# Performance work log

Hardware: AMD Instinct MI355X
Metric: run time of the kernel (lower is better)

The kernel has to match this reference:

```python
import jax, jax.numpy as jnp
import numpy as np

D = 256
H = 8
HD = D // H  # 32
EPS = 1e-5


def _ln(x, g, b):
    m = jnp.mean(x, axis=-1, keepdims=True)
    v = jnp.var(x, axis=-1, keepdims=True)
    return (x - m) * jax.lax.rsqrt(v + EPS) * g + b


def setup_inputs() -> dict:
    key = jax.random.key(0)
    ks = jax.random.split(key, 30)
    B = 131072
    s = 0.05

    def w(k, shape, scale=s):
        return jax.random.normal(k, shape, dtype=jnp.float32) * scale

    inp = {
        'f24': w(ks[0], (B, D), 1.0),
        'f77': w(ks[1], (B, D), 1.0),
        'fx': w(ks[2], (B, D), 1.0),
        'norm_g': jnp.ones((D,), jnp.float32),
        'norm_b': jnp.zeros((D,), jnp.float32),
        'Wq24': w(ks[3], (D, D)), 'bq24': w(ks[4], (D,)),
        'Wk24': w(ks[5], (D, D)), 'bk24': w(ks[6], (D,)),
        'Wv24': w(ks[7], (D, D)), 'bv24': w(ks[8], (D,)),
        'Wq77': w(ks[9], (D, D)), 'bq77': w(ks[10], (D,)),
        'Wk77': w(ks[11], (D, D)), 'bk77': w(ks[12], (D,)),
        'Wv77': w(ks[13], (D, D)), 'bv77': w(ks[14], (D,)),
        'Wqx': w(ks[15], (D, D)), 'bqx': w(ks[16], (D,)),
        'Wkx': w(ks[17], (D, D)), 'bkx': w(ks[18], (D,)),
        'Wvx': w(ks[19], (D, D)), 'bvx': w(ks[20], (D,)),
        'Wout': w(ks[21], (D, D)), 'bout': w(ks[22], (D,)),
        'radar_w': jnp.ones((3,), jnp.float32),
        'W1': w(ks[23], (D, 4 * D)), 'b1': w(ks[24], (4 * D,)),
        'W2': w(ks[25], (4 * D, D)), 'b2': w(ks[26], (D,)),
        'fnorm_g': jnp.ones((D,), jnp.float32),
        'fnorm_b': jnp.zeros((D,), jnp.float32),
    }
    return inp


def reference(f24, f77, fx, norm_g, norm_b,
              Wq24, bq24, Wk24, bk24, Wv24, bv24,
              Wq77, bq77, Wk77, bk77, Wv77, bv77,
              Wqx, bqx, Wkx, bkx, Wvx, bvx,
              Wout, bout, radar_w, W1, b1, W2, b2,
              fnorm_g, fnorm_b):
    B = f24.shape[0]
    residual = (f24 + f77 + fx) / 3.0
    n24 = _ln(f24, norm_g, norm_b)
    n77 = _ln(f77, norm_g, norm_b)
    nx = _ln(fx, norm_g, norm_b)

    def proj(x, W, b):
        return (x @ W + b).reshape(B, H, HD)

    q24 = proj(n24, Wq24, bq24); k24 = proj(n24, Wk24, bk24); v24 = proj(n24, Wv24, bv24)
    q77 = proj(n77, Wq77, bq77); k77 = proj(n77, Wk77, bk77); v77 = proj(n77, Wv77, bv77)
    qx = proj(nx, Wqx, bqx); kx = proj(nx, Wkx, bkx); vx = proj(nx, Wvx, bvx)

    scale = HD ** (-0.5)

    def att(q, ka, kb):  # [B,H,H] each
        a = jnp.einsum('bhd,bgd->bhg', q, ka) * scale
        b_ = jnp.einsum('bhd,bgd->bhg', q, kb) * scale
        # softmax across the two radar sources (stacked dim), NOT over keys
        return jax.nn.softmax(jnp.stack([a, b_], axis=1), axis=1)

    attn_24 = att(q24, k77, kx)
    attn_77 = att(q77, k24, kx)
    attn_x = att(qx, k24, k77)

    def mix(p, va, vb):  # [B,2,H,H] x [B,H,HD] -> [B, D]
        o = jnp.einsum('bhg,bgd->bhd', p[:, 0], va) + jnp.einsum('bhg,bgd->bhd', p[:, 1], vb)
        return o.reshape(B, D)

    out_24 = mix(attn_24, v77, vx)
    out_77 = mix(attn_77, v24, vx)
    out_x = mix(attn_x, v24, v77)

    rw = jax.nn.softmax(radar_w, axis=0)
    fused = rw[0] * out_24 + rw[1] * out_77 + rw[2] * out_x
    fused = fused @ Wout + bout
    fused = fused + residual
    ff = jax.nn.gelu(fused @ W1 + b1, approximate=False) @ W2 + b2  # dropout = eval identity
    output = _ln(fused + ff, fnorm_g, fnorm_b)
    return output, rw
```

## Files before the change

### kernel.cpp

```cpp
#include <hip/hip_runtime.h>

#define DEV __device__ __forceinline__

typedef float f4_t __attribute__((ext_vector_type(4)));
typedef short v8s  __attribute__((ext_vector_type(8)));

DEV float lo16(unsigned int w){ return __uint_as_float(w << 16); }
DEV float hi16(unsigned int w){ return __uint_as_float(w & 0xffff0000u); }
DEV float b2f(unsigned short u){ return __uint_as_float((unsigned)u << 16); }
DEV unsigned short f2b(float f){
  unsigned int x = __float_as_uint(f);
  x += 0x7fffu + ((x >> 16) & 1u);
  return (unsigned short)(x >> 16);
}
DEV float geluf(float v){ return 0.5f * v * (1.0f + erff(v * 0.7071067811865475f)); }

DEV void gload_lds16(const unsigned short* g, unsigned short* l){
  __builtin_amdgcn_global_load_lds(
      (const __attribute__((address_space(1))) void*)g,
      (__attribute__((address_space(3))) void*)l, 16, 0, 0);
}

#define WAITV(n) asm volatile("s_waitcnt vmcnt(" #n ")" ::: "memory")
#define SBAR()  do{ __builtin_amdgcn_sched_barrier(0); \
                    asm volatile("s_barrier" ::: "memory"); \
                    __builtin_amdgcn_sched_barrier(0); }while(0)

__global__ void k_prep(
    const float* Wq24, const float* Wk24, const float* Wv24,
    const float* Wq77, const float* Wk77, const float* Wv77,
    const float* Wqx,  const float* Wkx,  const float* Wvx,
    const float* bq24, const float* bk24, const float* bv24,
    const float* bq77, const float* bk77, const float* bv77,
    const float* bqx,  const float* bkx,  const float* bvx,
    const float* Wout, const float* W1,   const float* W2,
    const float* radar_w,
    unsigned short* wt_cat, unsigned short* wout_t,
    unsigned short* w1_t, unsigned short* w2_t,
    float* bias_cat, float* rwbuf, float* out_tail)
{
  long idx = (long)blockIdx.x * blockDim.x + threadIdx.x;
  if (idx < 589824){
    int s = (int)(idx / 196608);
    int r = (int)(idx % 196608);
    int ng = r >> 8, k = r & 255;
    int which = ng >> 8, n = ng & 255;
    const float* src;
    switch (s*3 + which){
      case 0: src = Wq24; break;  case 1: src = Wk24; break;  case 2: src = Wv24; break;
      case 3: src = Wq77; break;  case 4: src = Wk77; break;  case 5: src = Wv77; break;
      case 6: src = Wqx;  break;  case 7: src = Wkx;  break;  default: src = Wvx; break;
    }
    wt_cat[idx] = f2b(src[k*256 + n]);
    return;
  }
  idx -= 589824;
  if (idx < 65536){ int n = (int)(idx >> 8), k = (int)(idx & 255);
    wout_t[idx] = f2b(Wout[k*256 + n]); return; }
  idx -= 65536;
  if (idx < 262144){ int n = (int)(idx >> 8), k = (int)(idx & 255);
    w1_t[idx] = f2b(W1[k*1024 + n]); return; }
  idx -= 262144;
  if (idx < 262144){ int n = (int)(idx >> 10), k = (int)(idx & 1023);
    w2_t[idx] = f2b(W2[k*256 + n]); return; }
  idx -= 262144;
  if (idx < 2304){
    int s = (int)(idx / 768), j = (int)(idx % 768);
    int which = j >> 8, jj = j & 255;
    const float* src;
    switch (s*3 + which){
      case 0: src = bq24; break;  case 1: src = bk24; break;  case 2: src = bv24; break;
      case 3: src = bq77; break;  case 4: src = bk77; break;  case 5: src = bv77; break;
      case 6: src = bqx;  break;  case 7: src = bkx;  break;  default: src = bvx; break;
    }
    bias_cat[idx] = src[jj]; return;
  }
  idx -= 2304;
  if (idx < 3){
    float w0 = radar_w[0], w1v = radar_w[1], w2v = radar_w[2];
    float m = fmaxf(w0, fmaxf(w1v, w2v));
    float e0 = __expf(w0-m), e1 = __expf(w1v-m), e2 = __expf(w2v-m);
    float inv = 1.0f/(e0+e1+e2);
    float rw = (idx==0 ? e0 : (idx==1 ? e1 : e2)) * inv;
    rwbuf[idx] = rw; out_tail[idx] = rw;
  }
}

__global__ __launch_bounds__(256) void k_ln3(
    const float* __restrict__ f24, const float* __restrict__ f77, const float* __restrict__ fx,
    const float* __restrict__ gg, const float* __restrict__ bb,
    unsigned short* __restrict__ nbuf, float* __restrict__ resid, int rows)
{
  int wid = threadIdx.x >> 6, lane = threadIdx.x & 63;
  long row = (long)blockIdx.x*4 + wid;
  long base = row*256 + lane*4;
  f4_t x0 = *(const f4_t*)(f24 + base);
  f4_t x1 = *(const f4_t*)(f77 + base);
  f4_t x2 = *(const f4_t*)(fx  + base);
  float s[3], q[3];
  s[0]=x0.x+x0.y+x0.z+x0.w;
  s[1]=x1.x+x1.y+x1.z+x1.w;
  s[2]=x2.x+x2.y+x2.z+x2.w;
  q[0]=fmaf(x0.x,x0.x,fmaf(x0.y,x0.y,fmaf(x0.z,x0.z,x0.w*x0.w)));
  q[1]=fmaf(x1.x,x1.x,fmaf(x1.y,x1.y,fmaf(x1.z,x1.z,x1.w*x1.w)));
  q[2]=fmaf(x2.x,x2.x,fmaf(x2.y,x2.y,fmaf(x2.z,x2.z,x2.w*x2.w)));
  #pragma unroll
  for (int m=1;m<64;m<<=1){
    #pragma unroll
    for (int j=0;j<3;j++){ s[j]+=__shfl_xor(s[j],m); q[j]+=__shfl_xor(q[j],m); }
  }
  f4_t G  = *(const f4_t*)(gg + lane*4);
  f4_t Bv = *(const f4_t*)(bb + lane*4);
  long strm = (long)rows*256;
  {
    float mean = s[0]*(1.0f/256.0f);
    float rstd = rsqrtf(q[0]*(1.0f/256.0f) - mean*mean + 1e-5f);
    ushort4 o;
    o.x=f2b((x0.x-mean)*rstd*G.x+Bv.x); o.y=f2b((x0.y-mean)*rstd*G.y+Bv.y);
    o.z=f2b((x0.z-mean)*rstd*G.z+Bv.z); o.w=f2b((x0.w-mean)*rstd*G.w+Bv.w);
    *(ushort4*)(nbuf + base) = o;
  }
  {
    float mean = s[1]*(1.0f/256.0f);
    float rstd = rsqrtf(q[1]*(1.0f/256.0f) - mean*mean + 1e-5f);
    ushort4 o;
    o.x=f2b((x1.x-mean)*rstd*G.x+Bv.x); o.y=f2b((x1.y-mean)*rstd*G.y+Bv.y);
    o.z=f2b((x1.z-mean)*rstd*G.z+Bv.z); o.w=f2b((x1.w-mean)*rstd*G.w+Bv.w);
    *(ushort4*)(nbuf + strm + base) = o;
  }
  {
    float mean = s[2]*(1.0f/256.0f);
    float rstd = rsqrtf(q[2]*(1.0f/256.0f) - mean*mean + 1e-5f);
    ushort4 o;
    o.x=f2b((x2.x-mean)*rstd*G.x+Bv.x); o.y=f2b((x2.y-mean)*rstd*G.y+Bv.y);
    o.z=f2b((x2.z-mean)*rstd*G.z+Bv.z); o.w=f2b((x2.w-mean)*rstd*G.w+Bv.w);
    *(ushort4*)(nbuf + 2*strm + base) = o;
  }
  f4_t rs;
  rs.x=(x0.x+x1.x+x2.x)*(1.0f/3.0f);
  rs.y=(x0.y+x1.y+x2.y)*(1.0f/3.0f);
  rs.z=(x0.z+x1.z+x2.z)*(1.0f/3.0f);
  rs.w=(x0.w+x1.w+x2.w)*(1.0f/3.0f);
  *(f4_t*)(resid + base) = rs;
}

template<int EPI>
__global__ __launch_bounds__(256,2) void k_gemm256(
    const unsigned short* __restrict__ A, const unsigned short* __restrict__ Bt,
    const float* __restrict__ bias,
    unsigned short* __restrict__ outH,
    long aBatch, long bBatch, long biasBatch, long oBatch, int ldOut,
    int tM, int tN, int tZ)
{
  __shared__ __align__(16) unsigned short As[2][128][64];
  __shared__ __align__(16) unsigned short Bs[2][128][64];
  int tid = threadIdx.x, wid = tid >> 6, lane = tid & 63;
  int wm = (wid >> 1)*64, wn = (wid & 1)*64;
  int lr = lane & 15, lk = lane >> 4;

  int total = tM*tN*tZ;
  int nT = (total - (int)blockIdx.x + (int)gridDim.x - 1) / (int)gridDim.x;
  if (nT <= 0) return;
  int G = nT*4;

  auto tileOf = [&](int j, long& m0, int& n0, int& z){
    int T = (int)blockIdx.x + j*(int)gridDim.x;
    int mt = T % tM; int rest = T / tM;
    int nt = rest % tN; z = rest / tN;
    m0 = (long)mt*128; n0 = nt*128;
  };

  auto stage = [&](int g){
    long m0; int n0, z;
    tileOf(g >> 2, m0, n0, z);
    int k0 = (g & 3)*64, bi = g & 1;
    const unsigned short* Ab = A  + (long)z*aBatch + m0*256;
    const unsigned short* Bb = Bt + (long)z*bBatch + (long)n0*256;
    #pragma unroll
    for (int i=0;i<4;i++){
      int c = (wid*4+i)*64 + lane;
      int r = c >> 3, sl = (c & 7) ^ (r & 7);
      gload_lds16(Ab + (long)r*256 + k0 + sl*8, &As[bi][0][0] + (long)(wid*4+i)*512);
      gload_lds16(Bb + (long)r*256 + k0 + sl*8, &Bs[bi][0][0] + (long)(wid*4+i)*512);
    }
  };

  const f4_t fz = {0.f,0.f,0.f,0.f};
  f4_t acc[4][4] = {};

  stage(0);
  for (int g=0; g<G; ++g){
    if (g+1 < G){ stage(g+1); WAITV(8); }
    else        { WAITV(0); }
    SBAR();
    int cur = g & 1;
    #pragma unroll
    for (int ks=0; ks<2; ++ks){
      v8s af[4], bfv[4];
      #pragma unroll
      for (int f=0; f<4; f++){
        int prA = wm + f*16 + lr;
        int prB = wn + f*16 + lr;
        int js  = ks*4 + lk;
        af[f]  = *(const v8s*)&As[cur][prA][(js ^ (prA & 7))*8];
        bfv[f] = *(const v8s*)&Bs[cur][prB][(js ^ (prB & 7))*8];
      }
      #pragma unroll
      for (int fm=0; fm<4; fm++)
        #pragma unroll
        for (int fn=0; fn<4; fn++)
          acc[fm][fn] = __builtin_amdgcn_mfma_f32_16x16x32_bf16(bfv[fn], af[fm], acc[fm][fn], 0,0,0);
    }
    if ((g & 3) == 3){
      long m0; int n0, z;
      tileOf(g >> 2, m0, n0, z);
      long zo = (long)z*oBatch;
      const float* bp = bias + (long)z*biasBatch;
      #pragma unroll
      for (int fm=0; fm<4; fm++){
        long gm = m0 + wm + fm*16 + lr;
        long rowo = zo + gm*(long)ldOut;
        #pragma unroll
        for (int fn=0; fn<4; fn++){
          int gn = n0 + wn + fn*16 + lk*4;
          f4_t bv = *(const f4_t*)(bp + gn);
          f4_t v = acc[fm][fn];
          v.x += bv.x; v.y += bv.y; v.z += bv.z; v.w += bv.w;
          ushort4 o; o.x=f2b(v.x); o.y=f2b(v.y); o.z=f2b(v.z); o.w=f2b(v.w);
          *(ushort4*)(outH + rowo + gn) = o;
          acc[fm][fn] = fz;
        }
      }
    }
    SBAR();
  }
}

__global__ __launch_bounds__(512,4) void k_attn(
    const unsigned short* __restrict__ qkv, const float* __restrict__ rwb,
    unsigned short* __restrict__ outA, int rows)
{
  __shared__ __align__(16) unsigned short L[2][8][72][32];
  int tid = threadIdx.x, wid = tid >> 6, lane = tid & 63;
  int nT = rows >> 3;
  int t0 = blockIdx.x;
  if (t0 >= nT) return;

  auto stage = [&](int b, int tile){
    long brow0 = (long)tile*8;
    unsigned short* Lb = &L[b][0][0][0];
    #pragma unroll
    for (int it=0; it<5; ++it){
      int cw = it*512 + wid*64;
      if (cw < 2304){
        int c = cw + lane;
        int row = c/288, rem = c - row*288;
        int s = rem/96,  cc  = rem - s*96;
        gload_lds16(qkv + ((long)s*rows + brow0 + row)*768 + cc*8,
                    Lb + (long)cw*8);
      }
    }
  };

  float rw0 = rwb[0], rw1 = rwb[1], rw2 = rwb[2];
  int h = lane >> 3, g = lane & 7;

  stage(0, t0);
  int pb = 0;
  for (int t = t0; t < nT; t += (int)gridDim.x){
    SBAR();
    int tn = t + (int)gridDim.x;
    if (tn < nT){ stage(pb^1, tn); WAITV(5); }
    else        { WAITV(0); }
    SBAR();

    const unsigned short* R = &L[pb][wid][0][0];
    float comb[32];
    #pragma unroll
    for (int i=0;i<32;i++) comb[i] = 0.0f;

    #pragma unroll
    for (int att=0; att<3; ++att){
      int qs  = att;
      int as_ = (att==0) ? 1 : 0;
      int bs_ = (att==2) ? 1 : 2;
      float rwv = (att==0) ? rw0 : ((att==1) ? rw1 : rw2);
      const unsigned short* qp  = R + (qs *24      + h)*32;
      const unsigned short* kap = R + (as_*24 + 8  + g)*32;
      const unsigned short* kbp = R + (bs_*24 + 8  + g)*32;
      float a0=0.f, a1=0.f, b0=0.f, b1=0.f;
      #pragma unroll
      for (int j=0;j<4;j++){
        uint4 qc  = *(const uint4*)(qp  + j*8);
        uint4 kac = *(const uint4*)(kap + j*8);
        uint4 kbc = *(const uint4*)(kbp + j*8);
        float* ap = (j&1) ? &a1 : &a0;
        float* bp = (j&1) ? &b1 : &b0;
        #define DOT2(QW,KA,KB) { float q0=lo16(QW), q1=hi16(QW); \
          *ap=fmaf(q0,lo16(KA),*ap); *ap=fmaf(q1,hi16(KA),*ap); \
          *bp=fmaf(q0,lo16(KB),*bp); *bp=fmaf(q1,hi16(KB),*bp); }
        DOT2(qc.x, kac.x, kbc.x) DOT2(qc.y, kac.y, kbc.y)
        DOT2(qc.z, kac.z, kbc.z) DOT2(qc.w, kac.w, kbc.w)
        #undef DOT2
      }
      float d  = ((b0+b1) - (a0+a1)) * 0.17677669529663689f;
      float p0 = 1.0f / (1.0f + __expf(d));
      float p1 = 1.0f - p0;
      float w0 = rwv * p0, w1 = rwv * p1;
      const unsigned short* vap = R + (as_*24 + 16 + g)*32;
      const unsigned short* vbp = R + (bs_*24 + 16 + g)*32;
      #pragma unroll
      for (int j=0;j<4;j++){
        uint4 va = *(const uint4*)(vap + j*8);
        uint4 vb = *(const uint4*)(vbp + j*8);
        #define MIX2(VA,VB,C0,C1) { \
          C0 = fmaf(w0, lo16(VA), fmaf(w1, lo16(VB), C0)); \
          C1 = fmaf(w0, hi16(VA), fmaf(w1, hi16(VB), C1)); }
        MIX2(va.x, vb.x, comb[j*8+0], comb[j*8+1])
        MIX2(va.y, vb.y, comb[j*8+2], comb[j*8+3])
        MIX2(va.z, vb.z, comb[j*8+4], comb[j*8+5])
        MIX2(va.w, vb.w, comb[j*8+6], comb[j*8+7])
        #undef MIX2
      }
    }

    float t16[16];
    { bool up = (lane & 4) != 0;
      #pragma unroll
      for (int i=0;i<16;i++){
        float send = up ? comb[i] : comb[16+i];
        float keep = up ? comb[16+i] : comb[i];
        t16[i] = keep + __shfl_xor(send, 4);
      } }
    float t8[8];
    { bool up = (lane & 2) != 0;
      #pragma unroll
      for (int i=0;i<8;i++){
        float send = up ? t16[i] : t16[8+i];
        float keep = up ? t16[8+i] : t16[i];
        t8[i] = keep + __shfl_xor(send, 2);
      } }
    float t4[4];
    { bool up = (lane & 1) != 0;
      #pragma unroll
      for (int i=0;i<4;i++){
        float send = up ? t8[i] : t8[4+i];
        float keep = up ? t8[4+i] : t8[i];
        t4[i] = keep + __shfl_xor(send, 1);
      } }

    long orow = (long)t*8 + wid;
    ushort4 o4;
    o4.x = f2b(t4[0]); o4.y = f2b(t4[1]); o4.z = f2b(t4[2]); o4.w = f2b(t4[3]);
    *(ushort4*)(outA + orow*256 + lane*4) = o4;
    pb ^= 1;
  }
}

__global__ __launch_bounds__(256,2) void k_back(
    const unsigned short* __restrict__ attn,
    const float* __restrict__ resid,
    const unsigned short* __restrict__ woutT,
    const unsigned short* __restrict__ w1T,
    const unsigned short* __restrict__ w2T,
    const float* __restrict__ bout, const float* __restrict__ b1,
    const float* __restrict__ b2,
    const float* __restrict__ fg, const float* __restrict__ fb,
    float* __restrict__ dout)
{
  __shared__ __align__(16) unsigned short FL[8192];
  __shared__ __align__(16) unsigned short STG[16384];
  __shared__ __align__(16) unsigned short R2[4096];
  int tid = threadIdx.x, wid = tid >> 6, lane = tid & 63;
  int lr = lane & 15, lk = lane >> 4;
  int wn = wid*64, wnB = wid*32;
  long m0 = (long)blockIdx.x * 32;

  f4_t accA[2][4] = {};
  for (int t=0; t<4; ++t){
    { int c = tid; int r = c>>3, sl = (c&7)^(r&7);
      gload_lds16(attn + (m0+r)*256 + t*64 + sl*8, R2 + c*8); }
    #pragma unroll
    for (int i=0;i<8;i++){ int c = i*256+tid; int r = c>>3, sl = (c&7)^(r&7);
      gload_lds16(woutT + (long)r*256 + t*64 + sl*8, STG + c*8); }
    __syncthreads();
    #pragma unroll
    for (int ks=0; ks<2; ++ks){
      v8s af[2], bf[4];
      #pragma unroll
      for (int f=0; f<2; f++){ int pr = f*16+lr;
        af[f] = *(const v8s*)(R2 + pr*64 + (((ks*4+lk) ^ (pr&7))*8)); }
      #pragma unroll
      for (int f=0; f<4; f++){ int pr = wn + f*16 + lr;
        bf[f] = *(const v8s*)(STG + pr*64 + (((ks*4+lk) ^ (pr&7))*8)); }
      #pragma unroll
      for (int fm=0; fm<2; fm++)
        #pragma unroll
        for (int fn=0; fn<4; fn++)
          accA[fm][fn] = __builtin_amdgcn_mfma_f32_16x16x32_bf16(bf[fn], af[fm], accA[fm][fn], 0,0,0);
    }
    __syncthreads();
  }
  #pragma unroll
  for (int fm=0; fm<2; fm++){
    int row = fm*16 + lr;
    #pragma unroll
    for (int fn=0; fn<4; fn++){
      int col = wn + fn*16 + lk*4;
      f4_t bv = *(const f4_t*)(bout + col);
      f4_t rv = *(const f4_t*)(resid + (m0+row)*256 + col);
      f4_t v = accA[fm][fn];
      v.x += bv.x + rv.x; v.y += bv.y + rv.y; v.z += bv.z + rv.z; v.w += bv.w + rv.w;
      ushort4 hh; hh.x=f2b(v.x); hh.y=f2b(v.y); hh.z=f2b(v.z); hh.w=f2b(v.w);
      int us = row*256 + (((col>>3) ^ (row&7))*8) + (col&7);
      *(ushort4*)(FL + us) = hh;
    }
  }
  __syncthreads();

  f4_t acc2[2][4] = {};
  for (int s=0; s<8; ++s){
    f4_t accH[2][2] = {};
    for (int t=0; t<4; ++t){
      #pragma unroll
      for (int i=0;i<4;i++){ int c = i*256+tid; int r = c>>3, sl = (c&7)^(r&7);
        gload_lds16(w1T + (long)(s*128+r)*256 + t*64 + sl*8, STG + c*8); }
      __syncthreads();
      #pragma unroll
      for (int ks=0; ks<2; ++ks){
        v8s af[2], bf[2];
        #pragma unroll
        for (int f=0; f<2; f++){ int pr = f*16+lr; int ku = t*8 + ks*4 + lk;
          af[f] = *(const v8s*)(FL + pr*256 + ((ku ^ (pr&7))*8)); }
        #pragma unroll
        for (int f=0; f<2; f++){ int pr = wnB + f*16 + lr;
          bf[f] = *(const v8s*)(STG + pr*64 + (((ks*4+lk) ^ (pr&7))*8)); }
        #pragma unroll
        for (int fm=0; fm<2; fm++)
          #pragma unroll
          for (int fn=0; fn<2; fn++)
            accH[fm][fn] = __builtin_amdgcn_mfma_f32_16x16x32_bf16(bf[fn], af[fm], accH[fm][fn], 0,0,0);
      }
      __syncthreads();
    }
    #pragma unroll
    for (int fm=0; fm<2; fm++){
      int row = fm*16 + lr;
      #pragma unroll
      for (int fn=0; fn<2; fn++){
        int col = wnB + fn*16 + lk*4;
        f4_t bv = *(const f4_t*)(b1 + s*128 + col);
        f4_t v = accH[fm][fn];
        v.x = geluf(v.x+bv.x); v.y = geluf(v.y+bv.y);
        v.z = geluf(v.z+bv.z); v.w = geluf(v.w+bv.w);
        ushort4 hh; hh.x=f2b(v.x); hh.y=f2b(v.y); hh.z=f2b(v.z); hh.w=f2b(v.w);
        int us = row*128 + (((col>>3) ^ (row&7))*8) + (col&7);
        *(ushort4*)(R2 + us) = hh;
      }
    }
    __syncthreads();
    for (int t=0; t<2; ++t){
      #pragma unroll
      for (int i=0;i<8;i++){ int c = i*256+tid; int r = c>>3, sl = (c&7)^(r&7);
        gload_lds16(w2T + (long)r*1024 + s*128 + t*64 + sl*8, STG + c*8); }
      __syncthreads();
      #pragma unroll
      for (int ks=0; ks<2; ++ks){
        v8s af[2], bf[4];
        #pragma unroll
        for (int f=0; f<2; f++){ int pr = f*16+lr; int ku = t*8 + ks*4 + lk;
          af[f] = *(const v8s*)(R2 + pr*128 + ((ku ^ (pr&7))*8)); }
        #pragma unroll
        for (int f=0; f<4; f++){ int pr = wn + f*16 + lr;
          bf[f] = *(const v8s*)(STG + pr*64 + (((ks*4+lk) ^ (pr&7))*8)); }
        #pragma unroll
        for (int fm=0; fm<2; fm++)
          #pragma unroll
          for (int fn=0; fn<4; fn++)
            acc2[fm][fn] = __builtin_amdgcn_mfma_f32_16x16x32_bf16(bf[fn], af[fm], acc2[fm][fn], 0,0,0);
      }
      __syncthreads();
    }
  }

  f4_t vv[2][4];
  float ps[2], pq[2];
  #pragma unroll
  for (int fm=0; fm<2; fm++){
    int row = fm*16 + lr;
    ps[fm] = 0.0f; pq[fm] = 0.0f;
    #pragma unroll
    for (int fn=0; fn<4; fn++){
      int col = wn + fn*16 + lk*4;
      f4_t bv = *(const f4_t*)(b2 + col);
      int us = row*256 + (((col>>3) ^ (row&7))*8) + (col&7);
      ushort4 fh = *(const ushort4*)(FL + us);
      f4_t v = acc2[fm][fn];
      v.x += bv.x + b2f(fh.x); v.y += bv.y + b2f(fh.y);
      v.z += bv.z + b2f(fh.z); v.w += bv.w + b2f(fh.w);
      vv[fm][fn] = v;
      ps[fm] += v.x+v.y+v.z+v.w;
      pq[fm] += v.x*v.x + v.y*v.y + v.z*v.z + v.w*v.w;
    }
    ps[fm] += __shfl_xor(ps[fm], 16); ps[fm] += __shfl_xor(ps[fm], 32);
    pq[fm] += __shfl_xor(pq[fm], 16); pq[fm] += __shfl_xor(pq[fm], 32);
  }
  float* PS = (float*)R2;
  float* PQ = (float*)R2 + 128;
  if (lk == 0){
    #pragma unroll
    for (int fm=0; fm<2; fm++){ int row = fm*16+lr;
      PS[row*4 + wid] = ps[fm]; PQ[row*4 + wid] = pq[fm]; }
  }
  __syncthreads();
  #pragma unroll
  for (int fm=0; fm<2; fm++){
    int row = fm*16 + lr;
    f4_t sv = *(const f4_t*)(PS + row*4);
    f4_t qv = *(const f4_t*)(PQ + row*4);
    float S = sv.x+sv.y+sv.z+sv.w, Q = qv.x+qv.y+qv.z+qv.w;
    float mean = S*(1.0f/256.0f);
    float rstd = rsqrtf(Q*(1.0f/256.0f) - mean*mean + 1e-5f);
    #pragma unroll
    for (int fn=0; fn<4; fn++){
      int col = wn + fn*16 + lk*4;
      f4_t G = *(const f4_t*)(fg + col);
      f4_t Bb = *(const f4_t*)(fb + col);
      f4_t v = vv[fm][fn], o;
      o.x = (v.x-mean)*rstd*G.x + Bb.x;
      o.y = (v.y-mean)*rstd*G.y + Bb.y;
      o.z = (v.z-mean)*rstd*G.z + Bb.z;
      o.w = (v.w-mean)*rstd*G.w + Bb.w;
      *(f4_t*)(dout + (m0+row)*256 + col) = o;
    }
  }
}

extern "C" void kernel_launch(void* const* d_in, const int* in_sizes, int n_in,
                              void* d_out, int out_size, void* d_ws, size_t ws_size,
                              hipStream_t stream)
{
  const float* f24    = (const float*)d_in[0];
  const float* f77    = (const float*)d_in[1];
  const float* fx     = (const float*)d_in[2];
  const float* norm_g = (const float*)d_in[3];
  const float* norm_b = (const float*)d_in[4];
  const float* Wq24 = (const float*)d_in[5];  const float* bq24 = (const float*)d_in[6];
  const float* Wk24 = (const float*)d_in[7];  const float* bk24 = (const float*)d_in[8];
  const float* Wv24 = (const float*)d_in[9];  const float* bv24 = (const float*)d_in[10];
  const float* Wq77 = (const float*)d_in[11]; const float* bq77 = (const float*)d_in[12];
  const float* Wk77 = (const float*)d_in[13]; const float* bk77 = (const float*)d_in[14];
  const float* Wv77 = (const float*)d_in[15]; const float* bv77 = (const float*)d_in[16];
  const float* Wqx  = (const float*)d_in[17]; const float* bqx  = (const float*)d_in[18];
  const float* Wkx  = (const float*)d_in[19]; const float* bkx  = (const float*)d_in[20];
  const float* Wvx  = (const float*)d_in[21]; const float* bvx  = (const float*)d_in[22];
  const float* Wout = (const float*)d_in[23]; const float* bout = (const float*)d_in[24];
  const float* radar_w = (const float*)d_in[25];
  const float* W1 = (const float*)d_in[26];   const float* b1 = (const float*)d_in[27];
  const float* W2 = (const float*)d_in[28];   const float* b2 = (const float*)d_in[29];
  const float* fnorm_g = (const float*)d_in[30];
  const float* fnorm_b = (const float*)d_in[31];

  const long Brows = (long)in_sizes[0] / 256;
  float* dout = (float*)d_out;
  char* ws = (char*)d_ws;

  size_t off = 0;
  auto A_ = [&](size_t b){ size_t o = off; off = (off + b + 255) & ~(size_t)255; return o; };
  size_t oWT = A_((size_t)3*768*256*2);
  size_t oWO = A_((size_t)65536*2);
  size_t oW1 = A_((size_t)262144*2);
  size_t oW2 = A_((size_t)262144*2);
  size_t oBC = A_((size_t)2304*4);
  size_t oRW = A_(256);
  size_t fixedEnd = off;

  unsigned short* WT_CAT = (unsigned short*)(ws + oWT);
  unsigned short* WOUT_T = (unsigned short*)(ws + oWO);
  unsigned short* W1_T   = (unsigned short*)(ws + oW1);
  unsigned short* W2_T   = (unsigned short*)(ws + oW2);
  float*          BIASC  = (float*)(ws + oBC);
  float*          RW     = (float*)(ws + oRW);

  const size_t PER_ROW = 7168;
  if (ws_size <= fixedEnd + 512) return;
  long maxR = (long)((ws_size - fixedEnd - 256) / PER_ROW);
  maxR &= ~127L;
  if (maxR < 128) return;
  long Rc = maxR < 16384 ? maxR : 16384;
  if (Rc > Brows) Rc = Brows;
  long nch = (Brows + Rc - 1) / Rc;
  Rc = ((Brows + nch - 1) / nch + 127) & ~127L;

  size_t chunkBase = (fixedEnd + 255) & ~(size_t)255;
  char* NB_B = ws + chunkBase;
  char* RS_B = NB_B + (size_t)1536*Rc;
  char* QK_B = RS_B + (size_t)1024*Rc;

  {
    long total = 589824 + 65536 + 262144 + 262144 + 2304 + 3;
    int blocks = (int)((total + 255) / 256);
    k_prep<<<blocks, 256, 0, stream>>>(
        Wq24, Wk24, Wv24, Wq77, Wk77, Wv77, Wqx, Wkx, Wvx,
        bq24, bk24, bv24, bq77, bk77, bv77, bqx, bkx, bvx,
        Wout, W1, W2, radar_w,
        WT_CAT, WOUT_T, W1_T, W2_T, BIASC, RW, dout + (size_t)Brows*256);
  }

  for (long row0 = 0; row0 < Brows; row0 += Rc){
    long rows = Brows - row0 < Rc ? Brows - row0 : Rc;
    unsigned short* NBUF   = (unsigned short*)NB_B;
    float*          RESID  = (float*)RS_B;
    unsigned short* QKV    = (unsigned short*)QK_B;
    unsigned short* ATTN   = (unsigned short*)NB_B;

    int tM = (int)(rows/128);

    k_ln3<<<(int)(rows/4), 256, 0, stream>>>(
        f24 + row0*256, f77 + row0*256, fx + row0*256,
        norm_g, norm_b, NBUF, RESID, (int)rows);

    { int tiles = tM*6*3; int grid = tiles < 512 ? tiles : 512;
      k_gemm256<0><<<grid, 256, 0, stream>>>(
          NBUF, WT_CAT, BIASC, QKV,
          rows*256L, 768L*256, 768L, rows*768L, 768, tM, 6, 3); }

    { int nTa = (int)(rows/8); int ga = nTa < 512 ? nTa : 512;
      k_attn<<<ga, 512, 0, stream>>>(QKV, RW, ATTN, (int)rows); }

    k_back<<<(int)(rows/32), 256, 0, stream>>>(
        ATTN, RESID, WOUT_T, W1_T, W2_T,
        bout, b1, b2, fnorm_g, fnorm_b, dout + row0*256);
  }
}
```

Baseline: 1.405 ms.

## Double-buffer weight staging in back kernel with a flattened pipelined loop

Rewrites the k_back MLP/out-projection kernel so global-to-LDS weight loads use two ping-pong buffers. The next tile is prefetched while the current tile runs its MFMAs, with vmcnt waits replacing full __syncthreads drains. The W1 and W2 phases are merged into a single 64-step loop, and the residual, bout and b1 loads are moved up front (b1 staged into LDS). This hides load latency at the cost of more LDS (about 62KB per block), which may reduce occupancy under launch_bounds(256,2). Narrower K-steps for Wout and W2 also mean more barriers per unit of work.

```diff
diff --git a/kernel.cpp b/kernel.cpp
--- a/kernel.cpp
+++ b/kernel.cpp
@@ -20,8 +20,14 @@
       (const __attribute__((address_space(1))) void*)g,
       (__attribute__((address_space(3))) void*)l, 16, 0, 0);
 }
+DEV void gload_any16(const void* g, void* l){
+  __builtin_amdgcn_global_load_lds(
+      (const __attribute__((address_space(1))) void*)g,
+      (__attribute__((address_space(3))) void*)l, 16, 0, 0);
+}
 
 #define WAITV(n) asm volatile("s_waitcnt vmcnt(" #n ")" ::: "memory")
+#define LGKM0()  asm volatile("s_waitcnt lgkmcnt(0)" ::: "memory")
 #define SBAR()  do{ __builtin_amdgcn_sched_barrier(0); \
                     asm volatile("s_barrier" ::: "memory"); \
                     __builtin_amdgcn_sched_barrier(0); }while(0)
@@ -369,37 +375,79 @@
     float* __restrict__ dout)
 {
   __shared__ __align__(16) unsigned short FL[8192];
-  __shared__ __align__(16) unsigned short STG[16384];
-  __shared__ __align__(16) unsigned short R2[4096];
+  __shared__ __align__(16) unsigned short STG[2][9216];
+  __shared__ __align__(16) unsigned short Hs[4096];
+  __shared__ __align__(16) float b1L[1024];
   int tid = threadIdx.x, wid = tid >> 6, lane = tid & 63;
   int lr = lane & 15, lk = lane >> 4;
   int wn = wid*64, wnB = wid*32;
   long m0 = (long)blockIdx.x * 32;
 
+  auto stageA = [&](int t){
+    unsigned short* Bb = &STG[t&1][0];
+    #pragma unroll
+    for (int it=0; it<4; ++it){
+      int c = it*256 + tid;
+      int r = c >> 2, sl = (c & 3) ^ (r & 3);
+      gload_lds16(woutT + (long)r*256 + t*32 + sl*8, Bb + (it*256 + wid*64)*8);
+    }
+    if (lane < 32){
+      int c = wid*32 + lane;
+      int r = c >> 2, sl = (c & 3) ^ (r & 3);
+      gload_lds16(attn + (m0 + r)*256 + t*32 + sl*8, Bb + 8192 + wid*256);
+    }
+  };
+  auto stageF = [&](int jn){
+    int s = jn >> 3, ph = (jn >> 2) & 1, t = jn & 3;
+    unsigned short* Bb = &STG[jn&1][0];
+    if (ph == 0){
+      #pragma unroll
+      for (int it=0; it<4; ++it){
+        int c = it*256 + tid;
+        int r = c >> 3, sl = (c & 7) ^ (r & 7);
+        gload_lds16(w1T + (long)(s*128 + r)*256 + t*64 + sl*8, Bb + (it*256 + wid*64)*8);
+      }
+    } else {
+      #pragma unroll
+      for (int it=0; it<4; ++it){
+        int c = it*256 + tid;
+        int r = c >> 2, sl = (c & 3) ^ (r & 3);
+        gload_lds16(w2T + (long)r*1024 + s*128 + t*32 + sl*8, Bb + (it*256 + wid*64)*8);
+      }
+    }
+  };
+
+  gload_any16(b1 + (wid*64 + lane)*4, b1L + wid*256);
+  stageA(0);
+  f4_t rv[2][4], bvv[4];
+  #pragma unroll
+  for (int fm=0; fm<2; fm++)
+    #pragma unroll
+    for (int fn=0; fn<4; fn++)
+      rv[fm][fn] = *(const f4_t*)(resid + (m0 + fm*16 + lr)*256 + wn + fn*16 + lk*4);
+  #pragma unroll
+  for (int fn=0; fn<4; fn++) bvv[fn] = *(const f4_t*)(bout + wn + fn*16 + lk*4);
+
   f4_t accA[2][4] = {};
-  for (int t=0; t<4; ++t){
-    { int c = tid; int r = c>>3, sl = (c&7)^(r&7);
-      gload_lds16(attn + (m0+r)*256 + t*64 + sl*8, R2 + c*8); }
-    #pragma unroll
-    for (int i=0;i<8;i++){ int c = i*256+tid; int r = c>>3, sl = (c&7)^(r&7);
-      gload_lds16(woutT + (long)r*256 + t*64 + sl*8, STG + c*8); }
-    __syncthreads();
-    #pragma unroll
-    for (int ks=0; ks<2; ++ks){
-      v8s af[2], bf[4];
-      #pragma unroll
-      for (int f=0; f<2; f++){ int pr = f*16+lr;
-        af[f] = *(const v8s*)(R2 + pr*64 + (((ks*4+lk) ^ (pr&7))*8)); }
-      #pragma unroll
-      for (int f=0; f<4; f++){ int pr = wn + f*16 + lr;
-        bf[f] = *(const v8s*)(STG + pr*64 + (((ks*4+lk) ^ (pr&7))*8)); }
-      #pragma unroll
-      for (int fm=0; fm<2; fm++)
-        #pragma unroll
-        for (int fn=0; fn<4; fn++)
-          accA[fm][fn] = __builtin_amdgcn_mfma_f32_16x16x32_bf16(bf[fn], af[fm], accA[fm][fn], 0,0,0);
-    }
-    __syncthreads();
+  for (int t=0; t<8; ++t){
+    if (t < 7){ stageA(t+1); WAITV(5); }
+    else      { WAITV(0); }
+    SBAR();
+    unsigned short* Bb = &STG[t&1][0];
+    unsigned short* Ab = Bb + 8192;
+    v8s af[2], bf[4];
+    #pragma unroll
+    for (int f=0; f<2; f++){ int pr = f*16 + lr;
+      af[f] = *(const v8s*)(Ab + pr*32 + ((lk ^ (pr&3))*8)); }
+    #pragma unroll
+    for (int f=0; f<4; f++){ int pr = wn + f*16 + lr;
+      bf[f] = *(const v8s*)(Bb + pr*32 + ((lk ^ (pr&3))*8)); }
+    #pragma unroll
+    for (int fm=0; fm<2; fm++)
+      #pragma unroll
+      for (int fn=0; fn<4; fn++)
+        accA[fm][fn] = __builtin_amdgcn_mfma_f32_16x16x32_bf16(bf[fn], af[fm], accA[fm][fn], 0,0,0);
+    SBAR();
   }
   #pragma unroll
   for (int fm=0; fm<2; fm++){
@@ -407,80 +455,75 @@
     #pragma unroll
     for (int fn=0; fn<4; fn++){
       int col = wn + fn*16 + lk*4;
-      f4_t bv = *(const f4_t*)(bout + col);
-      f4_t rv = *(const f4_t*)(resid + (m0+row)*256 + col);
       f4_t v = accA[fm][fn];
-      v.x += bv.x + rv.x; v.y += bv.y + rv.y; v.z += bv.z + rv.z; v.w += bv.w + rv.w;
+      v.x += bvv[fn].x + rv[fm][fn].x; v.y += bvv[fn].y + rv[fm][fn].y;
+      v.z += bvv[fn].z + rv[fm][fn].z; v.w += bvv[fn].w + rv[fm][fn].w;
       ushort4 hh; hh.x=f2b(v.x); hh.y=f2b(v.y); hh.z=f2b(v.z); hh.w=f2b(v.w);
       int us = row*256 + (((col>>3) ^ (row&7))*8) + (col&7);
       *(ushort4*)(FL + us) = hh;
     }
   }
-  __syncthreads();
-
-  f4_t acc2[2][4] = {};
-  for (int s=0; s<8; ++s){
-    f4_t accH[2][2] = {};
-    for (int t=0; t<4; ++t){
-      #pragma unroll
-      for (int i=0;i<4;i++){ int c = i*256+tid; int r = c>>3, sl = (c&7)^(r&7);
-        gload_lds16(w1T + (long)(s*128+r)*256 + t*64 + sl*8, STG + c*8); }
-      __syncthreads();
+  LGKM0();
+  SBAR();
+
+  f4_t acc2[2][4] = {}, accH[2][2] = {};
+  stageF(0);
+  for (int j=0; j<64; ++j){
+    if (j < 63){ stageF(j+1); WAITV(4); }
+    else       { WAITV(0); }
+    SBAR();
+    int s = j >> 3, ph = (j >> 2) & 1, t = j & 3;
+    unsigned short* Bb = &STG[j&1][0];
+    if (ph == 0){
       #pragma unroll
       for (int ks=0; ks<2; ++ks){
         v8s af[2], bf[2];
         #pragma unroll
-        for (int f=0; f<2; f++){ int pr = f*16+lr; int ku = t*8 + ks*4 + lk;
+        for (int f=0; f<2; f++){ int pr = f*16 + lr; int ku = t*8 + ks*4 + lk;
           af[f] = *(const v8s*)(FL + pr*256 + ((ku ^ (pr&7))*8)); }
         #pragma unroll
         for (int f=0; f<2; f++){ int pr = wnB + f*16 + lr;
-          bf[f] = *(const v8s*)(STG + pr*64 + (((ks*4+lk) ^ (pr&7))*8)); }
+          bf[f] = *(const v8s*)(Bb + pr*64 + (((ks*4+lk) ^ (pr&7))*8)); }
         #pragma unroll
         for (int fm=0; fm<2; fm++)
           #pragma unroll
           for (int fn=0; fn<2; fn++)
             accH[fm][fn] = __builtin_amdgcn_mfma_f32_16x16x32_bf16(bf[fn], af[fm], accH[fm][fn], 0,0,0);
       }
-      __syncthreads();
-    }
-    #pragma unroll
-    for (int fm=0; fm<2; fm++){
-      int row = fm*16 + lr;
-      #pragma unroll
-      for (int fn=0; fn<2; fn++){
-        int col = wnB + fn*16 + lk*4;
-        f4_t bv = *(const f4_t*)(b1 + s*128 + col);
-        f4_t v = accH[fm][fn];
-        v.x = geluf(v.x+bv.x); v.y = geluf(v.y+bv.y);
-        v.z = geluf(v.z+bv.z); v.w = geluf(v.w+bv.w);
-        ushort4 hh; hh.x=f2b(v.x); hh.y=f2b(v.y); hh.z=f2b(v.z); hh.w=f2b(v.w);
-        int us = row*128 + (((col>>3) ^ (row&7))*8) + (col&7);
-        *(ushort4*)(R2 + us) = hh;
-      }
-    }
-    __syncthreads();
-    for (int t=0; t<2; ++t){
-      #pragma unroll
-      for (int i=0;i<8;i++){ int c = i*256+tid; int r = c>>3, sl = (c&7)^(r&7);
-        gload_lds16(w2T + (long)r*1024 + s*128 + t*64 + sl*8, STG + c*8); }
-      __syncthreads();
-      #pragma unroll
-      for (int ks=0; ks<2; ++ks){
-        v8s af[2], bf[4];
+      if (t == 3){
         #pragma unroll
-        for (int f=0; f<2; f++){ int pr = f*16+lr; int ku = t*8 + ks*4 + lk;
-          af[f] = *(const v8s*)(R2 + pr*128 + ((ku ^ (pr&7))*8)); }
+        for (int fm=0; fm<2; fm++){
+          int row = fm*16 + lr;
+          #pragma unroll
+          for (int fn=0; fn<2; fn++){
+            int col = wnB + fn*16 + lk*4;
+            f4_t bb = *(const f4_t*)(b1L + s*128 + col);
+            f4_t v = accH[fm][fn];
+            v.x = geluf(v.x+bb.x); v.y = geluf(v.y+bb.y);
+            v.z = geluf(v.z+bb.z); v.w = geluf(v.w+bb.w);
+            ushort4 hh; hh.x=f2b(v.x); hh.y=f2b(v.y); hh.z=f2b(v.z); hh.w=f2b(v.w);
+            int us = row*128 + (((col>>3) ^ (row&7))*8) + (col&7);
+            *(ushort4*)(Hs + us) = hh;
+            accH[fm][fn] = (f4_t){0.f,0.f,0.f,0.f};
+          }
+        }
+        LGKM0();
+      }
+    } else {
+      v8s af[2], bf[4];
+      #pragma unroll
+      for (int f=0; f<2; f++){ int pr = f*16 + lr; int ku = t*4 + lk;
+        af[f] = *(const v8s*)(Hs + pr*128 + ((ku ^ (pr&7))*8)); }
+      #pragma unroll
+      for (int f=0; f<4; f++){ int pr = wn + f*16 + lr;
+        bf[f] = *(const v8s*)(Bb + pr*32 + ((lk ^ (pr&3))*8)); }
+      #pragma unroll
+      for (int fm=0; fm<2; fm++)
         #pragma unroll
-        for (int f=0; f<4; f++){ int pr = wn + f*16 + lr;
-          bf[f] = *(const v8s*)(STG + pr*64 + (((ks*4+lk) ^ (pr&7))*8)); }
-        #pragma unroll
-        for (int fm=0; fm<2; fm++)
-          #pragma unroll
-          for (int fn=0; fn<4; fn++)
-            acc2[fm][fn] = __builtin_amdgcn_mfma_f32_16x16x32_bf16(bf[fn], af[fm], acc2[fm][fn], 0,0,0);
-      }
-      __syncthreads();
-    }
+        for (int fn=0; fn<4; fn++)
+          acc2[fm][fn] = __builtin_amdgcn_mfma_f32_16x16x32_bf16(bf[fn], af[fm], acc2[fm][fn], 0,0,0);
+    }
+    SBAR();
   }
 
   f4_t vv[2][4];
@@ -505,8 +548,8 @@
     ps[fm] += __shfl_xor(ps[fm], 16); ps[fm] += __shfl_xor(ps[fm], 32);
     pq[fm] += __shfl_xor(pq[fm], 16); pq[fm] += __shfl_xor(pq[fm], 32);
   }
-  float* PS = (float*)R2;
-  float* PQ = (float*)R2 + 128;
+  float* PS = (float*)&STG[0][0];
+  float* PQ = PS + 128;
   if (lk == 0){
     #pragma unroll
     for (int fm=0; fm<2; fm++){ int row = fm*16+lr;
@@ -525,12 +568,12 @@
     for (int fn=0; fn<4; fn++){
       int col = wn + fn*16 + lk*4;
       f4_t G = *(const f4_t*)(fg + col);
-      f4_t Bb = *(const f4_t*)(fb + col);
+      f4_t Bb2 = *(const f4_t*)(fb + col);
       f4_t v = vv[fm][fn], o;
-      o.x = (v.x-mean)*rstd*G.x + Bb.x;
-      o.y = (v.y-mean)*rstd*G.y + Bb.y;
-      o.z = (v.z-mean)*rstd*G.z + Bb.z;
-      o.w = (v.w-mean)*rstd*G.w + Bb.w;
+      o.x = (v.x-mean)*rstd*G.x + Bb2.x;
+      o.y = (v.y-mean)*rstd*G.y + Bb2.y;
+      o.z = (v.z-mean)*rstd*G.z + Bb2.z;
+      o.w = (v.w-mean)*rstd*G.w + Bb2.w;
       *(f4_t*)(dout + (m0+row)*256 + col) = o;
     }
   }
```

Measured after the change: 1.495 ms. 6.4% more time.
